# Kernel optimization log

Measured on AMD Instinct MI355X. Metric: run time of the kernel, lower is better.

The kernel has to match this reference:

```python
import jax, jax.numpy as jnp
import numpy as np

NPOINT, RADIUS, NSAMPLE = 1024, 0.2, 32
BN_EPS = 1e-5


def fps(xyz_bn3, npoint):
    # xyz_bn3: (B, N, 3) -> (B, npoint) int32 indices; starts from point 0 like the CUDA ext.
    def one(x):
        N = x.shape[0]
        def step(carry, _):
            dist, last = carry
            d = jnp.sum((x - x[last]) ** 2, axis=-1)
            dist = jnp.minimum(dist, d)
            nxt = jnp.argmax(dist).astype(jnp.int32)
            return (dist, nxt), nxt
        init = (jnp.full((N,), 1e10, dtype=x.dtype), jnp.int32(0))
        _, rest = jax.lax.scan(step, init, None, length=npoint - 1)
        return jnp.concatenate([jnp.zeros((1,), jnp.int32), rest])
    return jax.vmap(one)(xyz_bn3)


def ball_query(radius, nsample, xyz, new_xyz):
    # xyz: (B, N, 3), new_xyz: (B, S, 3) -> (B, S, nsample) int32
    # First nsample points within radius; pad slots with the first found index.
    N = xyz.shape[1]
    d2 = jnp.sum((new_xyz[:, :, None, :] - xyz[:, None, :, :]) ** 2, axis=-1)  # (B,S,N)
    ar = jnp.arange(N, dtype=jnp.int32)
    cand = jnp.where(d2 <= radius * radius, ar, N)
    idx = jnp.sort(cand, axis=-1)[..., :nsample]
    first = idx[..., :1]
    return jnp.where(idx == N, first, idx)


def group(features, idx):
    # features: (B, C, N), idx: (B, S, K) -> (B, C, S, K)
    return jax.vmap(lambda f, i: f[:, i])(features, idx)


def conv_bn_relu(x, w, b, g, bt, rm, rv):
    # x: (B, Cin, S, K); 1x1 conv + eval-mode BatchNorm + ReLU
    y = jnp.einsum('oc,bcsk->bosk', w, x) + b[:, None, None]
    y = g[:, None, None] * (y - rm[:, None, None]) * jax.lax.rsqrt(rv[:, None, None] + BN_EPS) + bt[:, None, None]
    return jax.nn.relu(y)


def setup_inputs() -> dict:
    key = jax.random.key(0)
    ks = jax.random.split(key, 16)
    B, N, D = 8, 4096, 64
    mlp = [64, 64, 128]
    cin = 3 + D
    inp = {
        'xyz': jax.random.uniform(ks[0], (B, 3, N), dtype=jnp.float32),
        'points': jax.random.normal(ks[1], (B, D, N), dtype=jnp.float32),
    }
    last = cin
    kidx = 2
    for i, co in enumerate(mlp):
        inp[f'w{i}'] = jax.random.normal(ks[kidx], (co, last), dtype=jnp.float32) * (1.0 / np.sqrt(last)); kidx += 1
        inp[f'b{i}'] = jax.random.normal(ks[kidx], (co,), dtype=jnp.float32) * 0.01; kidx += 1
        inp[f'g{i}'] = jax.random.uniform(ks[kidx], (co,), dtype=jnp.float32) + 0.5; kidx += 1
        inp[f'bt{i}'] = jax.random.normal(ks[kidx], (co,), dtype=jnp.float32) * 0.01; kidx += 1
        inp[f'rm{i}'] = jnp.zeros((co,), dtype=jnp.float32)
        inp[f'rv{i}'] = jnp.ones((co,), dtype=jnp.float32)
        last = co
    return inp


def reference(xyz, points, w0, b0, g0, bt0, rm0, rv0, w1, b1, g1, bt1, rm1, rv1, w2, b2, g2, bt2, rm2, rv2):
    xyz_t = jnp.transpose(xyz, (0, 2, 1))  # (B, N, 3)
    fps_idx = fps(xyz_t, NPOINT)  # (B, S)
    new_xyz = jax.vmap(lambda f, i: f[:, i])(xyz, fps_idx)  # (B, 3, S)
    idx = ball_query(RADIUS, NSAMPLE, xyz_t, jnp.transpose(new_xyz, (0, 2, 1)))  # (B, S, K)
    grouped_xyz = group(xyz, idx) - new_xyz[..., None]  # (B, 3, S, K)
    grouped_pts = group(points, idx)  # (B, D, S, K)
    feat = jnp.concatenate([grouped_xyz, grouped_pts], axis=1)  # (B, 3+D, S, K)
    feat = conv_bn_relu(feat, w0, b0, g0, bt0, rm0, rv0)
    feat = conv_bn_relu(feat, w1, b1, g1, bt1, rm1, rv1)
    feat = conv_bn_relu(feat, w2, b2, g2, bt2, rm2, rv2)
    new_features = jnp.max(feat, axis=-1)  # (B, 128, S)
    return new_xyz, new_features
```

## Files before the change

### kernel.cpp

```cpp
#include <hip/hip_runtime.h>
#include <cstdint>
#include <cstddef>

#define NPOINT 1024
#define NSAMPLE 32
#define BATCH 8
#define NPTS 4096
#define DFEAT 64
#define CIN 67
#define C1 64
#define C2 64
#define C3 128
#define BN_EPS 1e-5f

__device__ __forceinline__ float wave64_max_bcast(float v) {
    int x;
    x = __builtin_amdgcn_update_dpp(0, __float_as_int(v), 0x111, 0xf, 0xf, true);
    v = fmaxf(v, __int_as_float(x));
    x = __builtin_amdgcn_update_dpp(0, __float_as_int(v), 0x112, 0xf, 0xf, true);
    v = fmaxf(v, __int_as_float(x));
    x = __builtin_amdgcn_update_dpp(0, __float_as_int(v), 0x114, 0xf, 0xf, true);
    v = fmaxf(v, __int_as_float(x));
    x = __builtin_amdgcn_update_dpp(0, __float_as_int(v), 0x118, 0xf, 0xf, true);
    v = fmaxf(v, __int_as_float(x));
    x = __builtin_amdgcn_update_dpp(0, __float_as_int(v), 0x142, 0xf, 0xf, true);
    v = fmaxf(v, __int_as_float(x));
    x = __builtin_amdgcn_update_dpp(0, __float_as_int(v), 0x143, 0xf, 0xf, true);
    v = fmaxf(v, __int_as_float(x));
    return __int_as_float(__builtin_amdgcn_readlane(__float_as_int(v), 63));
}

__device__ __forceinline__ float max32_lane31(float v) {
    int iv = __float_as_int(v), x;
    x = __builtin_amdgcn_update_dpp(iv, iv, 0x111, 0xf, 0xf, false);
    v = fmaxf(v, __int_as_float(x)); iv = __float_as_int(v);
    x = __builtin_amdgcn_update_dpp(iv, iv, 0x112, 0xf, 0xf, false);
    v = fmaxf(v, __int_as_float(x)); iv = __float_as_int(v);
    x = __builtin_amdgcn_update_dpp(iv, iv, 0x114, 0xf, 0xf, false);
    v = fmaxf(v, __int_as_float(x)); iv = __float_as_int(v);
    x = __builtin_amdgcn_update_dpp(iv, iv, 0x118, 0xf, 0xf, false);
    v = fmaxf(v, __int_as_float(x)); iv = __float_as_int(v);
    x = __builtin_amdgcn_update_dpp(iv, iv, 0x142, 0xf, 0xf, false);
    v = fmaxf(v, __int_as_float(x));
    return v;
}

__global__ __launch_bounds__(512) void fps_kernel(const float* __restrict__ xyz,
                                                  float* __restrict__ dout) {
    const int b = blockIdx.x;
    const float* xb = xyz + (size_t)b * 3 * NPTS;
    float* ox = dout + (size_t)b * 3 * NPOINT;

    __shared__ float sx[NPTS], sy[NPTS], sz[NPTS];
    __shared__ unsigned long long redk[2][8];

    const int t = threadIdx.x;
    const int wv = t >> 6;
    for (int j = t; j < NPTS; j += 512) {
        sx[j] = xb[j];
        sy[j] = xb[NPTS + j];
        sz[j] = xb[2 * NPTS + j];
    }
    __syncthreads();

    constexpr int PT = NPTS / 512;
    float px[PT], py[PT], pz[PT], dist[PT];
    const int base = t * PT;
#pragma unroll
    for (int u = 0; u < PT; ++u) {
        px[u] = sx[base + u];
        py[u] = sy[base + u];
        pz[u] = sz[base + u];
        dist[u] = 1e10f;
    }

    int last = 0;
    float o0x = 0.f, o0y = 0.f, o0z = 0.f;
    float o1x = 0.f, o1y = 0.f, o1z = 0.f;

    for (int s = 1; s < NPOINT; ++s) {
        const float cx = sx[last], cy = sy[last], cz = sz[last];
        if (s - 1 == t)       { o0x = cx; o0y = cy; o0z = cz; }
        if (s - 1 == t + 512) { o1x = cx; o1y = cy; o1z = cz; }

        float bv = 0.0f;
#pragma unroll
        for (int u = 0; u < PT; ++u) {
            float dx = __fsub_rn(px[u], cx);
            float dy = __fsub_rn(py[u], cy);
            float dz = __fsub_rn(pz[u], cz);
            float d = __fadd_rn(__fadd_rn(__fmul_rn(dx, dx), __fmul_rn(dy, dy)),
                                __fmul_rn(dz, dz));
            float nd = fminf(dist[u], d);
            dist[u] = nd;
            bv = fmaxf(bv, nd);
        }
        const float wmax = wave64_max_bcast(bv);
        int li = 0;
        if (bv == wmax) {
#pragma unroll
            for (int u = PT - 1; u >= 0; --u)
                if (dist[u] == wmax) li = base + u;
        }
        const unsigned long long m = __ballot(bv == wmax);
        const int fl = __builtin_ctzll(m);
        const int wbi = __builtin_amdgcn_readlane(li, fl);

        if ((t & 63) == 0) {
            redk[s & 1][wv] =
                ((unsigned long long)__float_as_uint(wmax) << 32) |
                (unsigned)(0xFFFFFFFFu - (unsigned)wbi);
        }
        __syncthreads();
        unsigned long long gk = redk[s & 1][0];
#pragma unroll
        for (int w = 1; w < 8; ++w) {
            unsigned long long k2 = redk[s & 1][w];
            if (k2 > gk) gk = k2;
        }
        last = (int)(0xFFFFFFFFu - (unsigned)(gk & 0xFFFFFFFFull));
    }

    {
        const float cx = sx[last], cy = sy[last], cz = sz[last];
        if (t == 511) { o1x = cx; o1y = cy; o1z = cz; }
    }

    ox[t] = o0x;
    ox[NPOINT + t] = o0y;
    ox[2 * NPOINT + t] = o0z;
    ox[512 + t] = o1x;
    ox[NPOINT + 512 + t] = o1y;
    ox[2 * NPOINT + 512 + t] = o1z;
}

__global__ __launch_bounds__(256) void layer1_pts_kernel(
    const float* __restrict__ pts, const float* __restrict__ w0,
    float* __restrict__ A) {
    __shared__ float sp[64][65];
    __shared__ float sw[64][65];
    const int b = blockIdx.x >> 6;
    const int n0 = (blockIdx.x & 63) * 64;
    const int t = threadIdx.x;
    const int tn = t & 63, tq = t >> 6;
    const float* pb = pts + (size_t)b * DFEAT * NPTS;
#pragma unroll
    for (int i = 0; i < 16; ++i) {
        int c = i * 4 + tq;
        sp[c][tn] = pb[(size_t)c * NPTS + n0 + tn];
    }
#pragma unroll
    for (int i = 0; i < 16; ++i) {
        int o = i * 4 + tq;
        sw[o][tn] = w0[o * CIN + 3 + tn];
    }
    __syncthreads();

    float* An = A + ((size_t)b * NPTS + n0 + tn) * DFEAT;
#pragma unroll
    for (int i = 0; i < 16; ++i) {
        const int o = tq * 16 + i;
        float a0 = 0.f, a1 = 0.f, a2 = 0.f, a3 = 0.f;
#pragma unroll
        for (int c = 0; c < 64; c += 4) {
            a0 = fmaf(sw[o][c], sp[c][tn], a0);
            a1 = fmaf(sw[o][c + 1], sp[c + 1][tn], a1);
            a2 = fmaf(sw[o][c + 2], sp[c + 2][tn], a2);
            a3 = fmaf(sw[o][c + 3], sp[c + 3][tn], a3);
        }
        An[o] = (a0 + a1) + (a2 + a3);
    }
}

__global__ __launch_bounds__(256) void ballquery_kernel(const float* __restrict__ xyz,
                                                        const float* __restrict__ dout,
                                                        int* __restrict__ idx) {
    const int wv = threadIdx.x >> 6, lane = threadIdx.x & 63;
    const int sg = blockIdx.x * 4 + wv;
    const int b = sg / NPOINT, s = sg % NPOINT;
    const float* xb = xyz + (size_t)b * 3 * NPTS;
    const float* nx = dout + (size_t)b * 3 * NPOINT;
    const float cx = nx[s], cy = nx[NPOINT + s], cz = nx[2 * NPOINT + s];
    int* ob = idx + (size_t)sg * NSAMPLE;
    const float r2 = 0.04f;
    const unsigned long long lmask_lt = ((unsigned long long)1 << lane) - 1;

    int cnt = 0;
    int first = -1;
    for (int tch = 0; tch < NPTS / 64 && cnt < NSAMPLE; ++tch) {
        const int j = tch * 64 + lane;
        float dx = __fsub_rn(cx, xb[j]);
        float dy = __fsub_rn(cy, xb[NPTS + j]);
        float dz = __fsub_rn(cz, xb[2 * NPTS + j]);
        float d2 = __fadd_rn(__fadd_rn(__fmul_rn(dx, dx), __fmul_rn(dy, dy)),
                             __fmul_rn(dz, dz));
        const bool in = (d2 <= r2);
        const unsigned long long mask = __ballot(in);
        if (first < 0 && mask)
            first = tch * 64 + __builtin_ctzll(mask);
        if (in) {
            const int pos = cnt + __builtin_popcountll(mask & lmask_lt);
            if (pos < NSAMPLE) ob[pos] = j;
        }
        cnt += __builtin_popcountll(mask);
    }
    if (lane == 0) {
        for (int r = cnt; r < NSAMPLE; ++r) ob[r] = first;
    }
}

template <int MODE>
__global__ __launch_bounds__(256) void mlp_kernel(
    const float* __restrict__ xyz, const float* __restrict__ pts,
    const float* __restrict__ A, const int* __restrict__ idx,
    const float* __restrict__ dnew,
    const float* __restrict__ w0, const float* __restrict__ b0,
    const float* __restrict__ g0, const float* __restrict__ bt0,
    const float* __restrict__ rm0, const float* __restrict__ rv0,
    const float* __restrict__ w1, const float* __restrict__ b1,
    const float* __restrict__ g1, const float* __restrict__ bt1,
    const float* __restrict__ rm1, const float* __restrict__ rv1,
    const float* __restrict__ w2, const float* __restrict__ b2,
    const float* __restrict__ g2, const float* __restrict__ bt2,
    const float* __restrict__ rm2, const float* __restrict__ rv2,
    float* __restrict__ outf) {
    __shared__ float ylds[64][256];
    const int t = threadIdx.x;
    const int k = t & 31, sl = t >> 5;
    const int b = blockIdx.x >> 7;
    const int s = (blockIdx.x & 127) * 8 + sl;
    const int p = idx[((size_t)(b * NPOINT + s)) * NSAMPLE + k];

    const float* xb = xyz + (size_t)b * 3 * NPTS;
    const float* nx = dnew + (size_t)b * 3 * NPOINT;

    const float gx = xb[p] - nx[s];
    const float gy = xb[NPTS + p] - nx[NPOINT + s];
    const float gz = xb[2 * NPTS + p] - nx[2 * NPOINT + s];

    if (MODE == 1) {
        const float* Arow = A + ((size_t)b * NPTS + p) * DFEAT;
        for (int og = 0; og < C1; og += 4) {
            const float4 av = *(const float4*)(Arow + og);
#pragma unroll
            for (int u = 0; u < 4; ++u) {
                const int o = og + u;
                const float avu = (u == 0) ? av.x : (u == 1) ? av.y
                                 : (u == 2) ? av.z : av.w;
                const float* wr = w0 + o * CIN;
                float acc = fmaf(wr[0], gx,
                            fmaf(wr[1], gy, fmaf(wr[2], gz, avu)));
                float sc = g0[o] * rsqrtf(rv0[o] + BN_EPS);
                float y = fmaf(sc, acc + b0[o] - rm0[o], bt0[o]);
                ylds[o][t] = fmaxf(y, 0.f);
            }
        }
    } else {
        float x[CIN];
        x[0] = gx; x[1] = gy; x[2] = gz;
        const float* pb = pts + (size_t)b * DFEAT * NPTS + p;
#pragma unroll
        for (int c = 0; c < DFEAT; ++c) x[3 + c] = pb[(size_t)c * NPTS];
        for (int o = 0; o < C1; ++o) {
            const float* wr = w0 + o * CIN;
            float a0 = 0.f, a1 = 0.f, a2 = 0.f, a3 = 0.f;
#pragma unroll
            for (int c = 0; c < 64; c += 4) {
                a0 = fmaf(wr[c], x[c], a0);
                a1 = fmaf(wr[c + 1], x[c + 1], a1);
                a2 = fmaf(wr[c + 2], x[c + 2], a2);
                a3 = fmaf(wr[c + 3], x[c + 3], a3);
            }
            a0 = fmaf(wr[64], x[64], a0);
            a1 = fmaf(wr[65], x[65], a1);
            a2 = fmaf(wr[66], x[66], a2);
            float acc = (a0 + a1) + (a2 + a3);
            float sc = g0[o] * rsqrtf(rv0[o] + BN_EPS);
            float y = fmaf(sc, acc + b0[o] - rm0[o], bt0[o]);
            ylds[o][t] = fmaxf(y, 0.f);
        }
    }
    __syncthreads();
    float x1[C1];
#pragma unroll
    for (int c = 0; c < C1; ++c) x1[c] = ylds[c][t];
    __syncthreads();

    for (int o = 0; o < C2; ++o) {
        const float* wr = w1 + o * C1;
        float a0 = 0.f, a1 = 0.f, a2 = 0.f, a3 = 0.f;
#pragma unroll
        for (int c = 0; c < C1; c += 4) {
            a0 = fmaf(wr[c], x1[c], a0);
            a1 = fmaf(wr[c + 1], x1[c + 1], a1);
            a2 = fmaf(wr[c + 2], x1[c + 2], a2);
            a3 = fmaf(wr[c + 3], x1[c + 3], a3);
        }
        float acc = (a0 + a1) + (a2 + a3);
        float sc = g1[o] * rsqrtf(rv1[o] + BN_EPS);
        float y = fmaf(sc, acc + b1[o] - rm1[o], bt1[o]);
        ylds[o][t] = fmaxf(y, 0.f);
    }
    __syncthreads();
    float x2[C2];
#pragma unroll
    for (int c = 0; c < C2; ++c) x2[c] = ylds[c][t];

    float* ob = outf + (size_t)b * C3 * NPOINT;
    for (int o = 0; o < C3; ++o) {
        const float* wr = w2 + o * C2;
        float a0 = 0.f, a1 = 0.f, a2 = 0.f, a3 = 0.f;
#pragma unroll
        for (int c = 0; c < C2; c += 4) {
            a0 = fmaf(wr[c], x2[c], a0);
            a1 = fmaf(wr[c + 1], x2[c + 1], a1);
            a2 = fmaf(wr[c + 2], x2[c + 2], a2);
            a3 = fmaf(wr[c + 3], x2[c + 3], a3);
        }
        float acc = (a0 + a1) + (a2 + a3);
        float sc = g2[o] * rsqrtf(rv2[o] + BN_EPS);
        float key = (sc >= 0.f) ? acc : -acc;
        float mred = max32_lane31(key);
        if (k == 31) {
            float asel = (sc >= 0.f) ? mred : -mred;
            float y = fmaf(sc, asel + b2[o] - rm2[o], bt2[o]);
            ob[(size_t)o * NPOINT + s] = fmaxf(y, 0.f);
        }
    }
}

extern "C" void kernel_launch(void* const* d_in, const int* in_sizes, int n_in,
                              void* d_out, int out_size, void* d_ws, size_t ws_size,
                              hipStream_t stream) {
    const float* xyz = (const float*)d_in[0];
    const float* pts = (const float*)d_in[1];
    const float* w0 = (const float*)d_in[2];
    const float* b0 = (const float*)d_in[3];
    const float* g0 = (const float*)d_in[4];
    const float* bt0 = (const float*)d_in[5];
    const float* rm0 = (const float*)d_in[6];
    const float* rv0 = (const float*)d_in[7];
    const float* w1 = (const float*)d_in[8];
    const float* b1 = (const float*)d_in[9];
    const float* g1 = (const float*)d_in[10];
    const float* bt1 = (const float*)d_in[11];
    const float* rm1 = (const float*)d_in[12];
    const float* rv1 = (const float*)d_in[13];
    const float* w2 = (const float*)d_in[14];
    const float* b2 = (const float*)d_in[15];
    const float* g2 = (const float*)d_in[16];
    const float* bt2 = (const float*)d_in[17];
    const float* rm2 = (const float*)d_in[18];
    const float* rv2 = (const float*)d_in[19];

    float* out = (float*)d_out;
    float* outf = out + (size_t)BATCH * 3 * NPOINT;

    const size_t idx_bytes = (size_t)BATCH * NPOINT * NSAMPLE * sizeof(int);
    const size_t idx_pad = (idx_bytes + 255) & ~(size_t)255;
    const size_t A_bytes = (size_t)BATCH * NPTS * DFEAT * sizeof(float);
    int* idx = (int*)d_ws;
    float* A = (float*)((char*)d_ws + idx_pad);
    const bool useA = ws_size >= idx_pad + A_bytes;

    fps_kernel<<<BATCH, 512, 0, stream>>>(xyz, out);
    if (useA) layer1_pts_kernel<<<BATCH * 64, 256, 0, stream>>>(pts, w0, A);
    ballquery_kernel<<<BATCH * NPOINT / 4, 256, 0, stream>>>(xyz, out, idx);
    if (useA) {
        mlp_kernel<1><<<BATCH * NPOINT / 8, 256, 0, stream>>>(
            xyz, pts, A, idx, out, w0, b0, g0, bt0, rm0, rv0, w1, b1, g1, bt1,
            rm1, rv1, w2, b2, g2, bt2, rm2, rv2, outf);
    } else {
        mlp_kernel<0><<<BATCH * NPOINT / 8, 256, 0, stream>>>(
            xyz, pts, A, idx, out, w0, b0, g0, bt0, rm0, rv0, w1, b1, g1, bt1,
            rm1, rv1, w2, b2, g2, bt2, rm2, rv2, outf);
    }
}
```

Baseline: 926.4 us.

## Fuse layer-1 precompute and BN folding into FPS launch, inline ball query into MLP

Merges the point-feature layer-1 GEMM and a new BN scale/shift precompute into the FPS launch as extra blocks, so they run alongside the serial FPS blocks instead of as separate launches. The ball query now runs inside the MLP kernel and writes neighbor indices to shared memory, which removes a kernel launch and the global idx round trip. BN parameters are folded once into scale and shift, so the MLP no longer does per-output rsqrt and extra loads. The trade-off is that the extra blocks now use 512 threads and the FPS-sized shared memory allocation, and the ball query scan adds latency at the start of each MLP block.

```diff
diff --git a/kernel.cpp b/kernel.cpp
--- a/kernel.cpp
+++ b/kernel.cpp
@@ -45,16 +45,81 @@
     return v;
 }
 
-__global__ __launch_bounds__(512) void fps_kernel(const float* __restrict__ xyz,
-                                                  float* __restrict__ dout) {
+__global__ __launch_bounds__(512) void fps_aux_kernel(
+    const float* __restrict__ xyz, float* __restrict__ dout,
+    const float* __restrict__ pts, const float* __restrict__ w0,
+    const float* __restrict__ b0, const float* __restrict__ g0,
+    const float* __restrict__ bt0, const float* __restrict__ rm0,
+    const float* __restrict__ rv0,
+    const float* __restrict__ b1, const float* __restrict__ g1,
+    const float* __restrict__ bt1, const float* __restrict__ rm1,
+    const float* __restrict__ rv1,
+    const float* __restrict__ b2, const float* __restrict__ g2,
+    const float* __restrict__ bt2, const float* __restrict__ rm2,
+    const float* __restrict__ rv2,
+    float* __restrict__ A, float* __restrict__ bn) {
+    __shared__ __align__(16) float smem[3 * NPTS + 32];
+    const int t = threadIdx.x;
+
+    if (blockIdx.x == BATCH) {
+        if (t < 64) {
+            float sc = g0[t] * rsqrtf(rv0[t] + BN_EPS);
+            bn[t] = sc;
+            bn[64 + t] = fmaf(sc, b0[t] - rm0[t], bt0[t]);
+        } else if (t < 128) {
+            int c = t - 64;
+            float sc = g1[c] * rsqrtf(rv1[c] + BN_EPS);
+            bn[128 + c] = sc;
+            bn[192 + c] = fmaf(sc, b1[c] - rm1[c], bt1[c]);
+        } else if (t < 256) {
+            int c = t - 128;
+            float sc = g2[c] * rsqrtf(rv2[c] + BN_EPS);
+            bn[256 + c] = sc;
+            bn[384 + c] = fmaf(sc, b2[c] - rm2[c], bt2[c]);
+        }
+        return;
+    }
+    if (blockIdx.x > BATCH) {
+        const int tb = blockIdx.x - BATCH - 1;
+        float (*sp)[65] = (float(*)[65])smem;
+        float (*sw)[65] = (float(*)[65])(smem + 64 * 65);
+        const int b = tb >> 6;
+        const int n0 = (tb & 63) * 64;
+        const int tn = t & 63, tq = t >> 6;
+        const float* pb = pts + (size_t)b * DFEAT * NPTS;
+#pragma unroll
+        for (int i = 0; i < 8; ++i) {
+            int r = i * 8 + tq;
+            sp[r][tn] = pb[(size_t)r * NPTS + n0 + tn];
+            sw[r][tn] = w0[r * CIN + 3 + tn];
+        }
+        __syncthreads();
+        float* An = A + ((size_t)b * NPTS + n0 + tn) * DFEAT;
+#pragma unroll
+        for (int i = 0; i < 8; ++i) {
+            const int o = tq * 8 + i;
+            float a0 = 0.f, a1 = 0.f, a2 = 0.f, a3 = 0.f;
+#pragma unroll
+            for (int c = 0; c < 64; c += 4) {
+                a0 = fmaf(sw[o][c], sp[c][tn], a0);
+                a1 = fmaf(sw[o][c + 1], sp[c + 1][tn], a1);
+                a2 = fmaf(sw[o][c + 2], sp[c + 2][tn], a2);
+                a3 = fmaf(sw[o][c + 3], sp[c + 3][tn], a3);
+            }
+            An[o] = (a0 + a1) + (a2 + a3);
+        }
+        return;
+    }
+
     const int b = blockIdx.x;
     const float* xb = xyz + (size_t)b * 3 * NPTS;
     float* ox = dout + (size_t)b * 3 * NPOINT;
 
-    __shared__ float sx[NPTS], sy[NPTS], sz[NPTS];
-    __shared__ unsigned long long redk[2][8];
-
-    const int t = threadIdx.x;
+    float* sx = smem;
+    float* sy = smem + NPTS;
+    float* sz = smem + 2 * NPTS;
+    unsigned long long (*redk)[8] = (unsigned long long(*)[8])(smem + 3 * NPTS);
+
     const int wv = t >> 6;
     for (int j = t; j < NPTS; j += 512) {
         sx[j] = xb[j];
@@ -132,44 +197,6 @@
     ox[512 + t] = o1x;
     ox[NPOINT + 512 + t] = o1y;
     ox[2 * NPOINT + 512 + t] = o1z;
-}
-
-__global__ __launch_bounds__(256) void layer1_pts_kernel(
-    const float* __restrict__ pts, const float* __restrict__ w0,
-    float* __restrict__ A) {
-    __shared__ float sp[64][65];
-    __shared__ float sw[64][65];
-    const int b = blockIdx.x >> 6;
-    const int n0 = (blockIdx.x & 63) * 64;
-    const int t = threadIdx.x;
-    const int tn = t & 63, tq = t >> 6;
-    const float* pb = pts + (size_t)b * DFEAT * NPTS;
-#pragma unroll
-    for (int i = 0; i < 16; ++i) {
-        int c = i * 4 + tq;
-        sp[c][tn] = pb[(size_t)c * NPTS + n0 + tn];
-    }
-#pragma unroll
-    for (int i = 0; i < 16; ++i) {
-        int o = i * 4 + tq;
-        sw[o][tn] = w0[o * CIN + 3 + tn];
-    }
-    __syncthreads();
-
-    float* An = A + ((size_t)b * NPTS + n0 + tn) * DFEAT;
-#pragma unroll
-    for (int i = 0; i < 16; ++i) {
-        const int o = tq * 16 + i;
-        float a0 = 0.f, a1 = 0.f, a2 = 0.f, a3 = 0.f;
-#pragma unroll
-        for (int c = 0; c < 64; c += 4) {
-            a0 = fmaf(sw[o][c], sp[c][tn], a0);
-            a1 = fmaf(sw[o][c + 1], sp[c + 1][tn], a1);
-            a2 = fmaf(sw[o][c + 2], sp[c + 2][tn], a2);
-            a3 = fmaf(sw[o][c + 3], sp[c + 3][tn], a3);
-        }
-        An[o] = (a0 + a1) + (a2 + a3);
-    }
 }
 
 __global__ __launch_bounds__(256) void ballquery_kernel(const float* __restrict__ xyz,
@@ -213,7 +240,7 @@
 __global__ __launch_bounds__(256) void mlp_kernel(
     const float* __restrict__ xyz, const float* __restrict__ pts,
     const float* __restrict__ A, const int* __restrict__ idx,
-    const float* __restrict__ dnew,
+    const float* __restrict__ dnew, const float* __restrict__ bn,
     const float* __restrict__ w0, const float* __restrict__ b0,
     const float* __restrict__ g0, const float* __restrict__ bt0,
     const float* __restrict__ rm0, const float* __restrict__ rv0,
@@ -225,14 +252,53 @@
     const float* __restrict__ rm2, const float* __restrict__ rv2,
     float* __restrict__ outf) {
     __shared__ float ylds[64][256];
+    __shared__ int sIdx[8][NSAMPLE];
     const int t = threadIdx.x;
     const int k = t & 31, sl = t >> 5;
     const int b = blockIdx.x >> 7;
-    const int s = (blockIdx.x & 127) * 8 + sl;
-    const int p = idx[((size_t)(b * NPOINT + s)) * NSAMPLE + k];
+    const int sg0 = (blockIdx.x & 127) * 8;
+    const int s = sg0 + sl;
 
     const float* xb = xyz + (size_t)b * 3 * NPTS;
     const float* nx = dnew + (size_t)b * 3 * NPOINT;
+
+    int p;
+    if (MODE == 1) {
+        const int w = t >> 6, lane = t & 63;
+        const unsigned long long lmask_lt = ((unsigned long long)1 << lane) - 1;
+        const float r2 = 0.04f;
+#pragma unroll
+        for (int q = 0; q < 2; ++q) {
+            const int sl2 = w * 2 + q;
+            const int s2 = sg0 + sl2;
+            const float cx = nx[s2], cy = nx[NPOINT + s2], cz = nx[2 * NPOINT + s2];
+            int cnt = 0, first = -1;
+            for (int tch = 0; tch < NPTS / 64 && cnt < NSAMPLE; ++tch) {
+                const int j = tch * 64 + lane;
+                float dx = __fsub_rn(cx, xb[j]);
+                float dy = __fsub_rn(cy, xb[NPTS + j]);
+                float dz = __fsub_rn(cz, xb[2 * NPTS + j]);
+                float d2 = __fadd_rn(__fadd_rn(__fmul_rn(dx, dx), __fmul_rn(dy, dy)),
+                                     __fmul_rn(dz, dz));
+                const bool in = (d2 <= r2);
+                const unsigned long long mask = __ballot(in);
+                if (first < 0 && mask)
+                    first = tch * 64 + __builtin_ctzll(mask);
+                if (in) {
+                    const int pos = cnt + __builtin_popcountll(mask & lmask_lt);
+                    if (pos < NSAMPLE) sIdx[sl2][pos] = j;
+                }
+                cnt += __builtin_popcountll(mask);
+            }
+            if (lane == 0) {
+                for (int r = cnt; r < NSAMPLE; ++r) sIdx[sl2][r] = first;
+            }
+        }
+        __syncthreads();
+        p = sIdx[sl][k];
+    } else {
+        p = idx[((size_t)(b * NPOINT + s)) * NSAMPLE + k];
+    }
 
     const float gx = xb[p] - nx[s];
     const float gy = xb[NPTS + p] - nx[NPOINT + s];
@@ -250,8 +316,7 @@
                 const float* wr = w0 + o * CIN;
                 float acc = fmaf(wr[0], gx,
                             fmaf(wr[1], gy, fmaf(wr[2], gz, avu)));
-                float sc = g0[o] * rsqrtf(rv0[o] + BN_EPS);
-                float y = fmaf(sc, acc + b0[o] - rm0[o], bt0[o]);
+                float y = fmaf(bn[o], acc, bn[64 + o]);
                 ylds[o][t] = fmaxf(y, 0.f);
             }
         }
@@ -297,8 +362,13 @@
             a3 = fmaf(wr[c + 3], x1[c + 3], a3);
         }
         float acc = (a0 + a1) + (a2 + a3);
-        float sc = g1[o] * rsqrtf(rv1[o] + BN_EPS);
-        float y = fmaf(sc, acc + b1[o] - rm1[o], bt1[o]);
+        float y;
+        if (MODE == 1) {
+            y = fmaf(bn[128 + o], acc, bn[192 + o]);
+        } else {
+            float sc = g1[o] * rsqrtf(rv1[o] + BN_EPS);
+            y = fmaf(sc, acc + b1[o] - rm1[o], bt1[o]);
+        }
         ylds[o][t] = fmaxf(y, 0.f);
     }
     __syncthreads();
@@ -318,12 +388,19 @@
             a3 = fmaf(wr[c + 3], x2[c + 3], a3);
         }
         float acc = (a0 + a1) + (a2 + a3);
-        float sc = g2[o] * rsqrtf(rv2[o] + BN_EPS);
+        float sc, sh;
+        if (MODE == 1) {
+            sc = bn[256 + o];
+            sh = bn[384 + o];
+        } else {
+            sc = g2[o] * rsqrtf(rv2[o] + BN_EPS);
+            sh = fmaf(sc, b2[o] - rm2[o], bt2[o]);
+        }
         float key = (sc >= 0.f) ? acc : -acc;
         float mred = max32_lane31(key);
         if (k == 31) {
             float asel = (sc >= 0.f) ? mred : -mred;
-            float y = fmaf(sc, asel + b2[o] - rm2[o], bt2[o]);
+            float y = fmaf(sc, asel, sh);
             ob[(size_t)o * NPOINT + s] = fmaxf(y, 0.f);
         }
     }
@@ -359,20 +436,26 @@
     const size_t idx_bytes = (size_t)BATCH * NPOINT * NSAMPLE * sizeof(int);
     const size_t idx_pad = (idx_bytes + 255) & ~(size_t)255;
     const size_t A_bytes = (size_t)BATCH * NPTS * DFEAT * sizeof(float);
+    const size_t bn_bytes = 640 * sizeof(float);
     int* idx = (int*)d_ws;
     float* A = (float*)((char*)d_ws + idx_pad);
-    const bool useA = ws_size >= idx_pad + A_bytes;
-
-    fps_kernel<<<BATCH, 512, 0, stream>>>(xyz, out);
-    if (useA) layer1_pts_kernel<<<BATCH * 64, 256, 0, stream>>>(pts, w0, A);
-    ballquery_kernel<<<BATCH * NPOINT / 4, 256, 0, stream>>>(xyz, out, idx);
+    float* bn = (float*)((char*)d_ws + idx_pad + A_bytes);
+    const bool useA = ws_size >= idx_pad + A_bytes + bn_bytes;
+
     if (useA) {
+        fps_aux_kernel<<<BATCH + 1 + BATCH * 64, 512, 0, stream>>>(
+            xyz, out, pts, w0, b0, g0, bt0, rm0, rv0, b1, g1, bt1, rm1, rv1,
+            b2, g2, bt2, rm2, rv2, A, bn);
         mlp_kernel<1><<<BATCH * NPOINT / 8, 256, 0, stream>>>(
-            xyz, pts, A, idx, out, w0, b0, g0, bt0, rm0, rv0, w1, b1, g1, bt1,
-            rm1, rv1, w2, b2, g2, bt2, rm2, rv2, outf);
+            xyz, pts, A, idx, out, bn, w0, b0, g0, bt0, rm0, rv0, w1, b1, g1,
+            bt1, rm1, rv1, w2, b2, g2, bt2, rm2, rv2, outf);
     } else {
+        fps_aux_kernel<<<BATCH, 512, 0, stream>>>(
+            xyz, out, pts, w0, b0, g0, bt0, rm0, rv0, b1, g1, bt1, rm1, rv1,
+            b2, g2, bt2, rm2, rv2, A, bn);
+        ballquery_kernel<<<BATCH * NPOINT / 4, 256, 0, stream>>>(xyz, out, idx);
         mlp_kernel<0><<<BATCH * NPOINT / 8, 256, 0, stream>>>(
-            xyz, pts, A, idx, out, w0, b0, g0, bt0, rm0, rv0, w1, b1, g1, bt1,
-            rm1, rv1, w2, b2, g2, bt2, rm2, rv2, outf);
-    }
-}
+            xyz, pts, A, idx, out, bn, w0, b0, g0, bt0, rm0, rv0, w1, b1, g1,
+            bt1, rm1, rv1, w2, b2, g2, bt2, rm2, rv2, outf);
+    }
+}
```

After: 971.4 us. +4.9%, slower.
